# Kernel tuning notes

Measured on AMD Instinct MI355X. Metric: run time of the kernel, lower is better.

The kernel has to match this reference:

```python
import jax, jax.numpy as jnp
import numpy as np

N0, N1, N2 = 400000, 100000, 20000   # source nodes per sampled layer; dst nodes are a prefix
E1, E2 = 1000000, 200000
IN, HID, HEADS, OUT = 128, 256, 4, 47
C = HID // HEADS
EPS = 1e-5
NEG_SLOPE = 0.2


def setup_inputs() -> dict:
    key = jax.random.key(0)
    ks = jax.random.split(key, 20)
    def rn(i, shape, s=0.1):
        return jax.random.normal(ks[i], shape, jnp.float32) * s
    inp = {}
    inp["x"] = jax.random.normal(ks[0], (N0, IN), jnp.float32)
    inp["src1"] = jax.random.randint(ks[1], (E1,), 0, N0, jnp.int32)
    inp["dst1"] = jax.random.randint(ks[2], (E1,), 0, N1, jnp.int32)
    inp["src2"] = jax.random.randint(ks[3], (E2,), 0, N1, jnp.int32)
    inp["dst2"] = jax.random.randint(ks[4], (E2,), 0, N2, jnp.int32)
    # layer 1 GAT + skip + BN
    inp["W1"] = rn(5, (IN, HID)); inp["a_src1"] = rn(6, (HEADS, C)); inp["a_dst1"] = rn(7, (HEADS, C))
    inp["b1"] = jnp.zeros((HID,), jnp.float32)
    inp["Wsk1"] = rn(8, (IN, HID)); inp["bsk1"] = jnp.zeros((HID,), jnp.float32)
    inp["g1"] = jnp.ones((HID,), jnp.float32); inp["be1"] = jnp.zeros((HID,), jnp.float32)
    # layer 2 GAT + skip + BN
    inp["W2"] = rn(9, (HID, HID)); inp["a_src2"] = rn(10, (HEADS, C)); inp["a_dst2"] = rn(11, (HEADS, C))
    inp["b2"] = jnp.zeros((HID,), jnp.float32)
    inp["Wsk2"] = rn(12, (HID, HID)); inp["bsk2"] = jnp.zeros((HID,), jnp.float32)
    inp["g2"] = jnp.ones((HID,), jnp.float32); inp["be2"] = jnp.zeros((HID,), jnp.float32)
    # MLP head
    inp["Wm1"] = rn(13, (HID, HID)); inp["bm1"] = jnp.zeros((HID,), jnp.float32)
    inp["gm"] = jnp.ones((HID,), jnp.float32); inp["bem"] = jnp.zeros((HID,), jnp.float32)
    inp["Wm2"] = rn(14, (HID, OUT)); inp["bm2"] = jnp.zeros((OUT,), jnp.float32)
    return inp


def batch_norm(x, gamma, beta):
    mu = jnp.mean(x, axis=0)
    var = jnp.mean(jnp.square(x - mu), axis=0)  # biased var, as torch BN training
    return (x - mu) * jax.lax.rsqrt(var + EPS) * gamma + beta


def edge_softmax(logits, dst, n_dst):
    # logits: [E, H]; softmax over incoming edges per destination node
    m = jax.ops.segment_max(logits, dst, num_segments=n_dst)
    m = jax.lax.stop_gradient(jnp.where(jnp.isfinite(m), m, 0.0))
    e = jnp.exp(logits - m[dst])
    s = jax.ops.segment_sum(e, dst, num_segments=n_dst)
    return e / (s[dst] + 1e-16)


def gat_layer(x, n_dst, src, dst, W, a_src, a_dst, b, Wsk, bsk, gamma, beta):
    # GATConv (PyG, shared src/dst linear since in_channels is int) on bipartite (x, x[:n_dst])
    xp = (x @ W).reshape(-1, HEADS, C)                       # [N, H, C]
    al_s = jnp.einsum('nhc,hc->nh', xp, a_src)               # [N, H]
    al_d = jnp.einsum('nhc,hc->nh', xp[:n_dst], a_dst)       # [n_dst, H]
    logits = jax.nn.leaky_relu(al_s[src] + al_d[dst], NEG_SLOPE)   # [E, H]
    alpha = edge_softmax(logits, dst, n_dst)                 # [E, H]
    msg = xp[src] * alpha[:, :, None]                        # [E, H, C]
    out = jax.ops.segment_sum(msg, dst, num_segments=n_dst).reshape(n_dst, HID) + b
    out = out + x[:n_dst] @ Wsk + bsk                        # skip connection
    return jax.nn.elu(batch_norm(out, gamma, beta))          # dropout omitted (eval)


def reference(x, src1, dst1, src2, dst2,
              W1, a_src1, a_dst1, b1, Wsk1, bsk1, g1, be1,
              W2, a_src2, a_dst2, b2, Wsk2, bsk2, g2, be2,
              Wm1, bm1, gm, bem, Wm2, bm2):
    h = gat_layer(x, N1, src1, dst1, W1, a_src1, a_dst1, b1, Wsk1, bsk1, g1, be1)
    h = gat_layer(h, N2, src2, dst2, W2, a_src2, a_dst2, b2, Wsk2, bsk2, g2, be2)
    # MLP head: Linear -> BN -> ReLU -> (Dropout) -> Linear
    h = jax.nn.relu(batch_norm(h @ Wm1 + bm1, gm, bem))
    return h @ Wm2 + bm2                                     # logits [N2, OUT]
```

## Files before the change

kernel.cpp:

```cpp
#include <hip/hip_runtime.h>
#include <math.h>

constexpr int kN0 = 400000, kN1 = 100000, kN2 = 20000;
constexpr int kE1 = 1000000, kE2 = 200000;
constexpr int kIN = 128, kHID = 256, kOUT = 47;
constexpr float kEPS = 1e-5f, kNEG = 0.2f;

#define DEV static __device__ __forceinline__

typedef __attribute__((ext_vector_type(8))) short short8;
typedef __attribute__((ext_vector_type(4))) float f32x4;

DEV float b2f(unsigned short u) { return __uint_as_float(((unsigned)u) << 16); }
DEV unsigned short f2bf(float f) {
    unsigned u = __float_as_uint(f);
    unsigned r = (u + 0x7fffu + ((u >> 16) & 1u)) >> 16;
    return (unsigned short)r;
}
DEV float lrelu(float v) { return v > 0.f ? v : kNEG * v; }

DEV void gload_lds16(const void* g, void* l) {
    __builtin_amdgcn_global_load_lds(
        (const __attribute__((address_space(1))) void*)g,
        (__attribute__((address_space(3))) void*)l, 16, 0, 0);
}

__global__ void zero_f32(float* __restrict__ p, int n) {
    int i = blockIdx.x * blockDim.x + threadIdx.x;
    int st = gridDim.x * blockDim.x;
    for (; i < n; i += st) p[i] = 0.f;
}

__global__ void prep_weights(const float* __restrict__ W1, const float* __restrict__ as1,
                             const float* __restrict__ ad1,
                             const float* __restrict__ W2, const float* __restrict__ as2,
                             const float* __restrict__ ad2,
                             const float* __restrict__ Wsk1, const float* __restrict__ Wsk2,
                             const float* __restrict__ Wm1,
                             unsigned short* __restrict__ v1t, unsigned short* __restrict__ v2t,
                             unsigned short* __restrict__ Wcat1t,
                             unsigned short* __restrict__ Wcat2t,
                             unsigned short* __restrict__ Wm1t) {
    int i = blockIdx.x * blockDim.x + threadIdx.x;
    if (i < 2048) {
        int j = i >> 7, k = i & 127;
        float s = 0.f;
        if (j < 8) {
            int h = j & 3;
            const float* a = (j >= 4) ? ad1 : as1;
            for (int c = 0; c < 64; ++c) s += W1[(size_t)k * 256 + h * 64 + c] * a[h * 64 + c];
        }
        v1t[i] = f2bf(s);
        return;
    }
    i -= 2048;
    if (i < 4096) {
        int j = i >> 8, k = i & 255;
        float s = 0.f;
        if (j < 8) {
            int h = j & 3;
            const float* a = (j >= 4) ? ad2 : as2;
            for (int c = 0; c < 64; ++c) s += W2[(size_t)k * 256 + h * 64 + c] * a[h * 64 + c];
        }
        v2t[i] = f2bf(s);
        return;
    }
    i -= 4096;
    if (i < 163840) {
        int n = i / 640, k = i % 640;
        float v;
        if (k < 512) { int h = k >> 7, kin = k & 127; v = ((n >> 6) == h) ? W1[(size_t)kin * 256 + n] : 0.f; }
        else v = Wsk1[(size_t)(k - 512) * 256 + n];
        Wcat1t[i] = f2bf(v);
        return;
    }
    i -= 163840;
    if (i < 327680) {
        int n = i / 1280, k = i % 1280;
        float v;
        if (k < 1024) { int h = k >> 8, kin = k & 255; v = ((n >> 6) == h) ? W2[(size_t)kin * 256 + n] : 0.f; }
        else v = Wsk2[(size_t)(k - 1024) * 256 + n];
        Wcat2t[i] = f2bf(v);
        return;
    }
    i -= 327680;
    if (i < 65536) {
        int n = i >> 8, k = i & 255;
        Wm1t[i] = f2bf(Wm1[(size_t)k * 256 + n]);
    }
}

__global__ __launch_bounds__(256) void conv_als_mfma(const float* __restrict__ x,
                                                     const unsigned short* __restrict__ v1t,
                                                     unsigned short* __restrict__ xb,
                                                     float* __restrict__ als,
                                                     float* __restrict__ ald) {
    int wid = threadIdx.x >> 6, lane = threadIdx.x & 63;
    int l15 = lane & 15, l4 = lane >> 4;
    short8 bfr[4];
    #pragma unroll
    for (int ks = 0; ks < 4; ++ks)
        bfr[ks] = *reinterpret_cast<const short8*>(&v1t[l15 * 128 + ks * 32 + l4 * 8]);

    const int ntile = kN0 / 16;
    int nw = gridDim.x * 4;
    for (int t = blockIdx.x * 4 + wid; t < ntile; t += nw) {
        int base = t * 16;
        int r = base + l15;
        f32x4 acc = (f32x4){0.f, 0.f, 0.f, 0.f};
        #pragma unroll
        for (int ks = 0; ks < 4; ++ks) {
            size_t o = (size_t)r * 128 + ks * 32 + l4 * 8;
            float4 xa = *reinterpret_cast<const float4*>(&x[o]);
            float4 xc = *reinterpret_cast<const float4*>(&x[o + 4]);
            short8 af;
            af[0] = (short)f2bf(xa.x); af[1] = (short)f2bf(xa.y);
            af[2] = (short)f2bf(xa.z); af[3] = (short)f2bf(xa.w);
            af[4] = (short)f2bf(xc.x); af[5] = (short)f2bf(xc.y);
            af[6] = (short)f2bf(xc.z); af[7] = (short)f2bf(xc.w);
            *reinterpret_cast<short8*>(&xb[o]) = af;
            acc = __builtin_amdgcn_mfma_f32_16x16x32_bf16(af, bfr[ks], acc, 0, 0, 0);
        }
        if (l15 < 8) {
            #pragma unroll
            for (int i = 0; i < 4; ++i) {
                int node = base + l4 * 4 + i;
                if (l15 < 4) als[(size_t)node * 4 + l15] = acc[i];
                else if (node < kN1) ald[(size_t)node * 4 + (l15 - 4)] = acc[i];
            }
        }
    }
}

__global__ __launch_bounds__(256) void bn_mfma(const unsigned short* __restrict__ X,
                                               const float* __restrict__ stats,
                                               const float* __restrict__ gamma,
                                               const float* __restrict__ beta,
                                               unsigned short* __restrict__ outb,
                                               const unsigned short* __restrict__ v2t,
                                               float* __restrict__ als,
                                               float* __restrict__ ald,
                                               int M, int Ndst) {
    __shared__ float smu[256], ssc[256], ssh[256];
    {
        int c = threadIdx.x;
        float invM = 1.f / (float)M;
        float mu = stats[c] * invM;
        float var = stats[256 + c] * invM - mu * mu;
        smu[c] = mu;
        ssc[c] = rsqrtf(var + kEPS) * gamma[c];
        ssh[c] = beta[c];
    }
    __syncthreads();

    int wid = threadIdx.x >> 6, lane = threadIdx.x & 63;
    int l15 = lane & 15, l4 = lane >> 4;
    short8 bfr[8];
    #pragma unroll
    for (int ks = 0; ks < 8; ++ks)
        bfr[ks] = *reinterpret_cast<const short8*>(&v2t[l15 * 256 + ks * 32 + l4 * 8]);

    const int ntile = M / 16;
    int nw = gridDim.x * 4;
    for (int t = blockIdx.x * 4 + wid; t < ntile; t += nw) {
        int base = t * 16;
        int r = base + l15;
        f32x4 acc = (f32x4){0.f, 0.f, 0.f, 0.f};
        #pragma unroll
        for (int ks = 0; ks < 8; ++ks) {
            int c0 = ks * 32 + l4 * 8;
            size_t o = (size_t)r * 256 + c0;
            short8 xr = *reinterpret_cast<const short8*>(&X[o]);
            float4 mua = *reinterpret_cast<const float4*>(&smu[c0]);
            float4 muc = *reinterpret_cast<const float4*>(&smu[c0 + 4]);
            float4 sca = *reinterpret_cast<const float4*>(&ssc[c0]);
            float4 scc = *reinterpret_cast<const float4*>(&ssc[c0 + 4]);
            float4 sha = *reinterpret_cast<const float4*>(&ssh[c0]);
            float4 shc = *reinterpret_cast<const float4*>(&ssh[c0 + 4]);
            float v[8];
            v[0] = (b2f((unsigned short)xr[0]) - mua.x) * sca.x + sha.x;
            v[1] = (b2f((unsigned short)xr[1]) - mua.y) * sca.y + sha.y;
            v[2] = (b2f((unsigned short)xr[2]) - mua.z) * sca.z + sha.z;
            v[3] = (b2f((unsigned short)xr[3]) - mua.w) * sca.w + sha.w;
            v[4] = (b2f((unsigned short)xr[4]) - muc.x) * scc.x + shc.x;
            v[5] = (b2f((unsigned short)xr[5]) - muc.y) * scc.y + shc.y;
            v[6] = (b2f((unsigned short)xr[6]) - muc.z) * scc.z + shc.z;
            v[7] = (b2f((unsigned short)xr[7]) - muc.w) * scc.w + shc.w;
            short8 af;
            #pragma unroll
            for (int i = 0; i < 8; ++i) {
                float tv = v[i] > 0.f ? v[i] : expm1f(v[i]);
                af[i] = (short)f2bf(tv);
            }
            *reinterpret_cast<short8*>(&outb[o]) = af;
            acc = __builtin_amdgcn_mfma_f32_16x16x32_bf16(af, bfr[ks], acc, 0, 0, 0);
        }
        if (l15 < 8) {
            #pragma unroll
            for (int i = 0; i < 4; ++i) {
                int node = base + l4 * 4 + i;
                if (l15 < 4) als[(size_t)node * 4 + l15] = acc[i];
                else if (node < Ndst) ald[(size_t)node * 4 + (l15 - 4)] = acc[i];
            }
        }
    }
}

__global__ void hist_both(const int* __restrict__ dst1, int* __restrict__ cnt1, int E1,
                          const int* __restrict__ dst2, int* __restrict__ cnt2, int E2) {
    int e = blockIdx.x * blockDim.x + threadIdx.x;
    if (e < E1) atomicAdd(&cnt1[dst1[e]], 1);
    else if (e - E1 < E2) atomicAdd(&cnt2[dst2[e - E1]], 1);
}

__global__ __launch_bounds__(256) void scan_block_both(const int* __restrict__ cnt1, int n1,
                                                       int* __restrict__ offs1, int* __restrict__ bsum1, int nb1,
                                                       const int* __restrict__ cnt2, int n2,
                                                       int* __restrict__ offs2, int* __restrict__ bsum2) {
    const int* counts; int n; int* offs; int* bsum; int b;
    if ((int)blockIdx.x < nb1) { counts = cnt1; n = n1; offs = offs1; bsum = bsum1; b = blockIdx.x; }
    else { counts = cnt2; n = n2; offs = offs2; bsum = bsum2; b = blockIdx.x - nb1; }
    __shared__ int sh[256];
    int tid = threadIdx.x;
    int base = b * 1024 + tid * 4;
    int c0 = (base + 0 < n) ? counts[base + 0] : 0;
    int c1 = (base + 1 < n) ? counts[base + 1] : 0;
    int c2 = (base + 2 < n) ? counts[base + 2] : 0;
    int c3 = (base + 3 < n) ? counts[base + 3] : 0;
    int tot = c0 + c1 + c2 + c3;
    sh[tid] = tot;
    __syncthreads();
    for (int o = 1; o < 256; o <<= 1) {
        int t = (tid >= o) ? sh[tid - o] : 0;
        __syncthreads();
        sh[tid] += t;
        __syncthreads();
    }
    int excl = sh[tid] - tot;
    if (base + 0 < n) offs[base + 0] = excl;
    if (base + 1 < n) offs[base + 1] = excl + c0;
    if (base + 2 < n) offs[base + 2] = excl + c0 + c1;
    if (base + 3 < n) offs[base + 3] = excl + c0 + c1 + c2;
    if (tid == 255) bsum[b] = sh[255];
}

__global__ __launch_bounds__(256) void scan_bsums_both(const int* __restrict__ bsum1,
                                                       int* __restrict__ bscan1, int nb1,
                                                       const int* __restrict__ bsum2,
                                                       int* __restrict__ bscan2, int nb2) {
    __shared__ int sh[256];
    int tid = threadIdx.x;
    int v = (tid < nb1) ? bsum1[tid] : 0;
    sh[tid] = v;
    __syncthreads();
    for (int o = 1; o < 256; o <<= 1) {
        int t = (tid >= o) ? sh[tid - o] : 0;
        __syncthreads();
        sh[tid] += t;
        __syncthreads();
    }
    if (tid < nb1) bscan1[tid] = sh[tid] - v;
    __syncthreads();
    int v2 = (tid < nb2) ? bsum2[tid] : 0;
    sh[tid] = v2;
    __syncthreads();
    for (int o = 1; o < 256; o <<= 1) {
        int t = (tid >= o) ? sh[tid - o] : 0;
        __syncthreads();
        sh[tid] += t;
        __syncthreads();
    }
    if (tid < nb2) bscan2[tid] = sh[tid] - v2;
}

__global__ void scan_add_both(int* __restrict__ offs1, const int* __restrict__ bscan1,
                              const int* __restrict__ cnt1, int n1,
                              int* __restrict__ offs2, const int* __restrict__ bscan2,
                              const int* __restrict__ cnt2, int n2) {
    int i = blockIdx.x * blockDim.x + threadIdx.x;
    if (i < n1) {
        int v = offs1[i] + bscan1[i >> 10];
        offs1[i] = v;
        if (i == n1 - 1) offs1[n1] = v + cnt1[i];
    } else {
        int j = i - n1;
        if (j < n2) {
            int v = offs2[j] + bscan2[j >> 10];
            offs2[j] = v;
            if (j == n2 - 1) offs2[n2] = v + cnt2[j];
        }
    }
}

__global__ void csr_scatter_w(const int* __restrict__ dst, const int* __restrict__ src,
                              const int* __restrict__ offs,
                              const float* __restrict__ als, const float* __restrict__ ald,
                              int* __restrict__ cur, int* __restrict__ srcs,
                              float4* __restrict__ wbuf, int E) {
    int e = blockIdx.x * blockDim.x + threadIdx.x;
    if (e >= E) return;
    int d = dst[e], s = src[e];
    int pos = offs[d] + atomicAdd(&cur[d], 1);
    srcs[pos] = s;
    float4 a = *reinterpret_cast<const float4*>(&als[(size_t)s * 4]);
    float4 b = *reinterpret_cast<const float4*>(&ald[(size_t)d * 4]);
    float4 w;
    w.x = expf(lrelu(a.x + b.x));
    w.y = expf(lrelu(a.y + b.y));
    w.z = expf(lrelu(a.z + b.z));
    w.w = expf(lrelu(a.w + b.w));
    wbuf[pos] = w;
}

template <bool OUTBF, bool STATS>
__global__ __launch_bounds__(256) void gemm_pipe(const unsigned short* __restrict__ A1, int K1,
                                                 const unsigned short* __restrict__ A2, int K2,
                                                 const unsigned short* __restrict__ Bt,
                                                 void* __restrict__ Cv,
                                                 const float* __restrict__ bias1,
                                                 const float* __restrict__ bias2,
                                                 float* __restrict__ stats,
                                                 int M, int N, int rs, int kwin) {
    __shared__ unsigned short SH[4][128 * 64];
    const int tid = threadIdx.x;
    const int wid = tid >> 6, lane = tid & 63;
    const int wr = wid >> 1, wc = wid & 1;
    const int l15 = lane & 15, l4 = lane >> 4;
    const int m0 = blockIdx.y * 128, n0 = blockIdx.x * 128;
    const int rsub = lane >> 3;
    const int kslot = (lane & 7) ^ rsub;
    const int KB = K1 + K2;
    const int nwin = kwin >> 6;
    const int nt = nwin + (K2 >> 6);
    const int wbase = n0 * rs;

    auto stage = [&](int buf, int t) {
        const unsigned short* Asrc; int ka, lda, gk;
        if (t < nwin) { gk = wbase + (t << 6); Asrc = A1; ka = gk; lda = K1; }
        else { int t2 = t - nwin; gk = K1 + (t2 << 6); Asrc = A2; ka = t2 << 6; lda = K2; }
        #pragma unroll
        for (int c = 0; c < 4; ++c) {
            int q = wid * 4 + c;
            int rowA = m0 + q * 8 + rsub; if (rowA > M - 1) rowA = M - 1;
            gload_lds16(Asrc + (size_t)rowA * lda + ka + kslot * 8, &SH[buf][q * 512]);
            int rowB = n0 + q * 8 + rsub;
            gload_lds16(Bt + (size_t)rowB * KB + gk + kslot * 8, &SH[2 + buf][q * 512]);
        }
    };

    f32x4 acc[4][4];
    #pragma unroll
    for (int i = 0; i < 4; ++i)
        #pragma unroll
        for (int j = 0; j < 4; ++j) acc[i][j] = (f32x4){0.f, 0.f, 0.f, 0.f};

    stage(0, 0);
    __syncthreads();
    for (int t = 0; t < nt; ++t) {
        if (t + 1 < nt) stage((t + 1) & 1, t + 1);
        int b = t & 1;
        short8 af[2][4], bf[2][4];
        #pragma unroll
        for (int kk = 0; kk < 2; ++kk) {
            #pragma unroll
            for (int mi = 0; mi < 4; ++mi) {
                int row = wr * 64 + mi * 16 + l15;
                af[kk][mi] = *reinterpret_cast<const short8*>(
                    &SH[b][row * 64 + (((kk * 4 + l4) ^ (row & 7)) << 3)]);
            }
            #pragma unroll
            for (int ni = 0; ni < 4; ++ni) {
                int row = wc * 64 + ni * 16 + l15;
                bf[kk][ni] = *reinterpret_cast<const short8*>(
                    &SH[2 + b][row * 64 + (((kk * 4 + l4) ^ (row & 7)) << 3)]);
            }
        }
        #pragma unroll
        for (int kk = 0; kk < 2; ++kk)
            #pragma unroll
            for (int mi = 0; mi < 4; ++mi)
                #pragma unroll
                for (int ni = 0; ni < 4; ++ni)
                    acc[mi][ni] = __builtin_amdgcn_mfma_f32_16x16x32_bf16(
                        af[kk][mi], bf[kk][ni], acc[mi][ni], 0, 0, 0);
        __syncthreads();
    }

    float csum[4] = {0.f, 0.f, 0.f, 0.f}, csq[4] = {0.f, 0.f, 0.f, 0.f};
    unsigned short* LB = (unsigned short*)SH;
    float* LF = (float*)SH;
    #pragma unroll
    for (int mi = 0; mi < 4; ++mi) {
        int lrow0 = wr * 64 + mi * 16 + l4 * 4;
        #pragma unroll
        for (int ni = 0; ni < 4; ++ni) {
            int lcol = wc * 64 + ni * 16 + l15;
            int col = n0 + lcol;
            float badd = 0.f;
            if (bias1) badd += bias1[col];
            if (bias2) badd += bias2[col];
            f32x4 v = acc[mi][ni];
            #pragma unroll
            for (int i = 0; i < 4; ++i) {
                float o = v[i] + badd;
                if (STATS && (m0 + lrow0 + i) < M) { csum[ni] += o; csq[ni] += o * o; }
                if (OUTBF) LB[(lrow0 + i) * 128 + lcol] = f2bf(o);
                else LF[(lrow0 + i) * 128 + lcol] = o;
            }
        }
    }
    if (STATS) {
        #pragma unroll
        for (int ni = 0; ni < 4; ++ni) {
            float s = csum[ni], q = csq[ni];
            s += __shfl_xor(s, 16, 64); q += __shfl_xor(q, 16, 64);
            s += __shfl_xor(s, 32, 64); q += __shfl_xor(q, 32, 64);
            if (l4 == 0) {
                int col = n0 + wc * 64 + ni * 16 + l15;
                atomicAdd(&stats[col], s);
                atomicAdd(&stats[256 + col], q);
            }
        }
    }
    __syncthreads();
    if (OUTBF) {
        unsigned short* Cb = (unsigned short*)Cv;
        #pragma unroll
        for (int it = 0; it < 8; ++it) {
            int lin = (it * 256 + tid) * 8;
            int r = lin >> 7, c0 = lin & 127;
            int gr = m0 + r;
            if (gr < M)
                *reinterpret_cast<short8*>(&Cb[(size_t)gr * N + n0 + c0]) =
                    *reinterpret_cast<const short8*>(&LB[lin]);
        }
    } else {
        float* Cf = (float*)Cv;
        #pragma unroll
        for (int it = 0; it < 16; ++it) {
            int lin = (it * 256 + tid) * 4;
            int r = lin >> 7, c0 = lin & 127;
            int gr = m0 + r;
            if (gr < M)
                *reinterpret_cast<float4*>(&Cf[(size_t)gr * N + n0 + c0]) =
                    *reinterpret_cast<const float4*>(&LF[lin]);
        }
    }
}

__global__ __launch_bounds__(256) void fused_agg1(const unsigned short* __restrict__ xb,
                                                  const float4* __restrict__ wbuf,
                                                  const int* __restrict__ srcs,
                                                  const int* __restrict__ offs,
                                                  unsigned short* __restrict__ Agg, int Ndst) {
    int d = blockIdx.x * 4 + (threadIdx.x >> 6);
    if (d >= Ndst) return;
    int lane = threadIdx.x & 63;
    int beg = offs[d], end = offs[d + 1];
    float ac[4][2] = {};
    float se0 = 0.f, se1 = 0.f, se2 = 0.f, se3 = 0.f;

    auto edge = [&](int i) {
        int s = srcs[i];
        float4 w = wbuf[i];
        unsigned xv = *reinterpret_cast<const unsigned*>(&xb[(size_t)s * 128 + lane * 2]);
        se0 += w.x; se1 += w.y; se2 += w.z; se3 += w.w;
        float fx = b2f((unsigned short)(xv & 0xffff));
        float fy = b2f((unsigned short)(xv >> 16));
        ac[0][0] = fmaf(w.x, fx, ac[0][0]); ac[0][1] = fmaf(w.x, fy, ac[0][1]);
        ac[1][0] = fmaf(w.y, fx, ac[1][0]); ac[1][1] = fmaf(w.y, fy, ac[1][1]);
        ac[2][0] = fmaf(w.z, fx, ac[2][0]); ac[2][1] = fmaf(w.z, fy, ac[2][1]);
        ac[3][0] = fmaf(w.w, fx, ac[3][0]); ac[3][1] = fmaf(w.w, fy, ac[3][1]);
    };
    int i = beg;
    for (; i + 4 <= end; i += 4) { edge(i); edge(i + 1); edge(i + 2); edge(i + 3); }
    for (; i < end; ++i) edge(i);

    float inv0 = 1.f / (se0 + 1e-16f), inv1 = 1.f / (se1 + 1e-16f);
    float inv2 = 1.f / (se2 + 1e-16f), inv3 = 1.f / (se3 + 1e-16f);
    unsigned short* row = Agg + (size_t)d * 512;
    ushort2 o;
    o.x = f2bf(ac[0][0] * inv0); o.y = f2bf(ac[0][1] * inv0);
    *reinterpret_cast<ushort2*>(&row[0 * 128 + lane * 2]) = o;
    o.x = f2bf(ac[1][0] * inv1); o.y = f2bf(ac[1][1] * inv1);
    *reinterpret_cast<ushort2*>(&row[1 * 128 + lane * 2]) = o;
    o.x = f2bf(ac[2][0] * inv2); o.y = f2bf(ac[2][1] * inv2);
    *reinterpret_cast<ushort2*>(&row[2 * 128 + lane * 2]) = o;
    o.x = f2bf(ac[3][0] * inv3); o.y = f2bf(ac[3][1] * inv3);
    *reinterpret_cast<ushort2*>(&row[3 * 128 + lane * 2]) = o;
}

__global__ __launch_bounds__(256) void fused_agg2(const unsigned short* __restrict__ hb,
                                                  const float4* __restrict__ wbuf,
                                                  const int* __restrict__ srcs,
                                                  const int* __restrict__ offs,
                                                  unsigned short* __restrict__ Agg, int Ndst) {
    int d = blockIdx.x * 4 + (threadIdx.x >> 6);
    if (d >= Ndst) return;
    int lane = threadIdx.x & 63;
    int beg = offs[d], end = offs[d + 1];
    float ac[4][4] = {};
    float se0 = 0.f, se1 = 0.f, se2 = 0.f, se3 = 0.f;

    auto edge = [&](int i) {
        int s = srcs[i];
        float4 w = wbuf[i];
        ushort4 xv = *reinterpret_cast<const ushort4*>(&hb[(size_t)s * 256 + lane * 4]);
        se0 += w.x; se1 += w.y; se2 += w.z; se3 += w.w;
        float f0 = b2f(xv.x), f1 = b2f(xv.y), f2 = b2f(xv.z), f3 = b2f(xv.w);
        ac[0][0] = fmaf(w.x, f0, ac[0][0]); ac[0][1] = fmaf(w.x, f1, ac[0][1]);
        ac[0][2] = fmaf(w.x, f2, ac[0][2]); ac[0][3] = fmaf(w.x, f3, ac[0][3]);
        ac[1][0] = fmaf(w.y, f0, ac[1][0]); ac[1][1] = fmaf(w.y, f1, ac[1][1]);
        ac[1][2] = fmaf(w.y, f2, ac[1][2]); ac[1][3] = fmaf(w.y, f3, ac[1][3]);
        ac[2][0] = fmaf(w.z, f0, ac[2][0]); ac[2][1] = fmaf(w.z, f1, ac[2][1]);
        ac[2][2] = fmaf(w.z, f2, ac[2][2]); ac[2][3] = fmaf(w.z, f3, ac[2][3]);
        ac[3][0] = fmaf(w.w, f0, ac[3][0]); ac[3][1] = fmaf(w.w, f1, ac[3][1]);
        ac[3][2] = fmaf(w.w, f2, ac[3][2]); ac[3][3] = fmaf(w.w, f3, ac[3][3]);
    };
    int i = beg;
    for (; i + 2 <= end; i += 2) { edge(i); edge(i + 1); }
    for (; i < end; ++i) edge(i);

    float inv[4] = {1.f / (se0 + 1e-16f), 1.f / (se1 + 1e-16f),
                    1.f / (se2 + 1e-16f), 1.f / (se3 + 1e-16f)};
    unsigned short* row = Agg + (size_t)d * 1024;
    #pragma unroll
    for (int h = 0; h < 4; ++h) {
        ushort4 o;
        o.x = f2bf(ac[h][0] * inv[h]); o.y = f2bf(ac[h][1] * inv[h]);
        o.z = f2bf(ac[h][2] * inv[h]); o.w = f2bf(ac[h][3] * inv[h]);
        *reinterpret_cast<ushort4*>(&row[h * 256 + lane * 4]) = o;
    }
}

template <int ACT, bool OUTBF>
__global__ __launch_bounds__(256) void bn_rows(const float* __restrict__ X,
                                               const float* __restrict__ stats,
                                               const float* __restrict__ gamma,
                                               const float* __restrict__ beta,
                                               void* __restrict__ out, int M) {
    int wid = threadIdx.x >> 6, lane = threadIdx.x & 63;
    int nw = gridDim.x * 4;
    float4 s4 = *reinterpret_cast<const float4*>(&stats[lane * 4]);
    float4 q4 = *reinterpret_cast<const float4*>(&stats[256 + lane * 4]);
    float4 g4 = *reinterpret_cast<const float4*>(&gamma[lane * 4]);
    float4 b4 = *reinterpret_cast<const float4*>(&beta[lane * 4]);
    float invM = 1.f / (float)M;
    float mu[4] = {s4.x * invM, s4.y * invM, s4.z * invM, s4.w * invM};
    float sc[4], sh_[4] = {b4.x, b4.y, b4.z, b4.w};
    {
        float g[4] = {g4.x, g4.y, g4.z, g4.w};
        float q[4] = {q4.x, q4.y, q4.z, q4.w};
        #pragma unroll
        for (int c = 0; c < 4; ++c) {
            float var = q[c] * invM - mu[c] * mu[c];
            sc[c] = rsqrtf(var + kEPS) * g[c];
        }
    }
    for (int row = blockIdx.x * 4 + wid; row < M; row += nw) {
        float4 xv = *reinterpret_cast<const float4*>(&X[(size_t)row * 256 + lane * 4]);
        float v[4] = {xv.x, xv.y, xv.z, xv.w};
        #pragma unroll
        for (int c = 0; c < 4; ++c) {
            float t = (v[c] - mu[c]) * sc[c] + sh_[c];
            if (ACT == 0) t = t > 0.f ? t : expm1f(t);
            else t = fmaxf(t, 0.f);
            v[c] = t;
        }
        if (OUTBF) {
            ushort4 o; o.x = f2bf(v[0]); o.y = f2bf(v[1]); o.z = f2bf(v[2]); o.w = f2bf(v[3]);
            *reinterpret_cast<ushort4*>(&((unsigned short*)out)[(size_t)row * 256 + lane * 4]) = o;
        } else {
            *reinterpret_cast<float4*>(&((float*)out)[(size_t)row * 256 + lane * 4]) =
                make_float4(v[0], v[1], v[2], v[3]);
        }
    }
}

template <bool ACCUM>
__global__ __launch_bounds__(256) void gemm64(const float* __restrict__ A,
                                              const float* __restrict__ B,
                                              float* __restrict__ Cmat,
                                              const float* __restrict__ bias1,
                                              const float* __restrict__ bias2,
                                              int M, int N, int K) {
    __shared__ float As[32][68];
    __shared__ float Bs[32][68];
    const int tid = threadIdx.x;
    const int tx = tid & 15, ty = tid >> 4;
    const int m0 = blockIdx.y * 64, n0 = blockIdx.x * 64;
    float acc[4][4] = {};

    for (int k0 = 0; k0 < K; k0 += 32) {
        #pragma unroll
        for (int t = 0; t < 2; ++t) {
            int i = tid + t * 256;
            int row = i >> 3;
            int kq = (i & 7) << 2;
            float4 v = make_float4(0.f, 0.f, 0.f, 0.f);
            int gr = m0 + row;
            if (gr < M) v = *reinterpret_cast<const float4*>(&A[(size_t)gr * K + k0 + kq]);
            As[kq + 0][row] = v.x; As[kq + 1][row] = v.y;
            As[kq + 2][row] = v.z; As[kq + 3][row] = v.w;
        }
        #pragma unroll
        for (int t = 0; t < 2; ++t) {
            int i = tid + t * 256;
            int kr = i >> 4;
            int cq = (i & 15) << 2;
            #pragma unroll
            for (int j = 0; j < 4; ++j) {
                int gc = n0 + cq + j;
                Bs[kr][cq + j] = (gc < N) ? B[(size_t)(k0 + kr) * N + gc] : 0.f;
            }
        }
        __syncthreads();
        #pragma unroll
        for (int kk = 0; kk < 32; ++kk) {
            float4 a4 = *reinterpret_cast<const float4*>(&As[kk][ty << 2]);
            float4 b4 = *reinterpret_cast<const float4*>(&Bs[kk][tx << 2]);
            float a[4] = {a4.x, a4.y, a4.z, a4.w};
            float b[4] = {b4.x, b4.y, b4.z, b4.w};
            #pragma unroll
            for (int i2 = 0; i2 < 4; ++i2)
                #pragma unroll
                for (int j = 0; j < 4; ++j)
                    acc[i2][j] = fmaf(a[i2], b[j], acc[i2][j]);
        }
        __syncthreads();
    }

    #pragma unroll
    for (int i2 = 0; i2 < 4; ++i2) {
        int row = m0 + (ty << 2) + i2;
        if (row >= M) continue;
        #pragma unroll
        for (int j = 0; j < 4; ++j) {
            int col = n0 + (tx << 2) + j;
            if (col >= N) continue;
            float v = acc[i2][j];
            if (bias1) v += bias1[col];
            if (bias2) v += bias2[col];
            size_t idx = (size_t)row * N + col;
            if (ACCUM) v += Cmat[idx];
            Cmat[idx] = v;
        }
    }
}

extern "C" void kernel_launch(void* const* d_in, const int* in_sizes, int n_in,
                              void* d_out, int out_size, void* d_ws, size_t ws_size,
                              hipStream_t stream) {
    (void)in_sizes; (void)n_in; (void)out_size; (void)ws_size;

    const float* x      = (const float*)d_in[0];
    const int*   src1   = (const int*)d_in[1];
    const int*   dst1   = (const int*)d_in[2];
    const int*   src2   = (const int*)d_in[3];
    const int*   dst2   = (const int*)d_in[4];
    const float* W1     = (const float*)d_in[5];
    const float* a_src1 = (const float*)d_in[6];
    const float* a_dst1 = (const float*)d_in[7];
    const float* b1     = (const float*)d_in[8];
    const float* Wsk1   = (const float*)d_in[9];
    const float* bsk1   = (const float*)d_in[10];
    const float* g1     = (const float*)d_in[11];
    const float* be1    = (const float*)d_in[12];
    const float* W2     = (const float*)d_in[13];
    const float* a_src2 = (const float*)d_in[14];
    const float* a_dst2 = (const float*)d_in[15];
    const float* b2     = (const float*)d_in[16];
    const float* Wsk2   = (const float*)d_in[17];
    const float* bsk2   = (const float*)d_in[18];
    const float* g2     = (const float*)d_in[19];
    const float* be2    = (const float*)d_in[20];
    const float* Wm1    = (const float*)d_in[21];
    const float* bm1    = (const float*)d_in[22];
    const float* gm     = (const float*)d_in[23];
    const float* bem    = (const float*)d_in[24];
    const float* Wm2    = (const float*)d_in[25];
    const float* bm2    = (const float*)d_in[26];

    float* ws = (float*)d_ws;
    size_t off = 0;
    auto alloc = [&](size_t n) { float* p = ws + off; off += n; return p; };
    unsigned short* xb    = (unsigned short*)alloc((size_t)kN0 * 128 / 2);
    unsigned short* Agg1  = (unsigned short*)alloc((size_t)kN1 * 512 / 2);
    unsigned short* Agg2  = (unsigned short*)alloc((size_t)kN2 * 1024 / 2);
    unsigned short* h1pre = (unsigned short*)alloc((size_t)kN1 * 256 / 2);
    unsigned short* h1b   = (unsigned short*)alloc((size_t)kN1 * 256 / 2);
    float* h2             = alloc((size_t)kN2 * 256);
    unsigned short* h2b   = (unsigned short*)alloc((size_t)kN2 * 256 / 2);
    float* h3             = alloc((size_t)kN2 * 256);
    unsigned short* Wcat1t = (unsigned short*)alloc(256 * 640 / 2);
    unsigned short* Wcat2t = (unsigned short*)alloc(256 * 1280 / 2);
    unsigned short* Wm1t   = (unsigned short*)alloc(256 * 256 / 2);
    unsigned short* v1t    = (unsigned short*)alloc(16 * 128 / 2);
    unsigned short* v2t    = (unsigned short*)alloc(16 * 256 / 2);
    float4* w1buf = (float4*)alloc((size_t)kE1 * 4);
    float4* w2buf = (float4*)alloc((size_t)kE2 * 4);
    float* als1 = alloc((size_t)kN0 * 4);
    float* ald1 = alloc((size_t)kN1 * 4);
    float* als2 = alloc((size_t)kN1 * 4);
    float* ald2 = alloc((size_t)kN2 * 4);
    float* zreg = alloc(1536 + kN1 + kN1 + kN2 + kN2);
    float* stats1 = zreg, *stats2 = zreg + 512, *stats3 = zreg + 1024;
    int* cnt1 = (int*)(zreg + 1536);
    int* cur1 = cnt1 + kN1;
    int* cnt2 = cur1 + kN1;
    int* cur2 = cnt2 + kN2;
    const int nzreg = 1536 + 2 * kN1 + 2 * kN2;
    int* srcs1  = (int*)alloc(kE1);
    int* offs1  = (int*)alloc(kN1 + 4);
    int* bsum1  = (int*)alloc(128);
    int* bscan1 = (int*)alloc(128);
    int* srcs2  = (int*)alloc(kE2);
    int* offs2  = (int*)alloc(kN2 + 4);
    int* bsum2  = (int*)alloc(128);
    int* bscan2 = (int*)alloc(128);

    hipStream_t st = stream;
    const int nb1 = (kN1 + 1023) / 1024;
    const int nb2 = (kN2 + 1023) / 1024;

    prep_weights<<<(563200 + 255) / 256, 256, 0, st>>>(W1, a_src1, a_dst1, W2, a_src2, a_dst2,
                                                       Wsk1, Wsk2, Wm1,
                                                       v1t, v2t, Wcat1t, Wcat2t, Wm1t);
    zero_f32<<<512, 256, 0, st>>>(zreg, nzreg);

    conv_als_mfma<<<2048, 256, 0, st>>>(x, v1t, xb, als1, ald1);

    hist_both<<<(kE1 + kE2 + 255) / 256, 256, 0, st>>>(dst1, cnt1, kE1, dst2, cnt2, kE2);
    scan_block_both<<<nb1 + nb2, 256, 0, st>>>(cnt1, kN1, offs1, bsum1, nb1, cnt2, kN2, offs2, bsum2);
    scan_bsums_both<<<1, 256, 0, st>>>(bsum1, bscan1, nb1, bsum2, bscan2, nb2);
    scan_add_both<<<(kN1 + kN2 + 255) / 256, 256, 0, st>>>(offs1, bscan1, cnt1, kN1,
                                                           offs2, bscan2, cnt2, kN2);
    csr_scatter_w<<<(kE1 + 255) / 256, 256, 0, st>>>(dst1, src1, offs1, als1, ald1,
                                                     cur1, srcs1, w1buf, kE1);

    fused_agg1<<<(kN1 + 3) / 4, 256, 0, st>>>(xb, w1buf, srcs1, offs1, Agg1, kN1);
    gemm_pipe<true, true><<<dim3(2, (kN1 + 127) / 128), 256, 0, st>>>(
        Agg1, 512, xb, 128, Wcat1t, h1pre, b1, bsk1, stats1, kN1, 256, 2, 256);
    bn_mfma<<<1024, 256, 0, st>>>(h1pre, stats1, g1, be1, h1b, v2t, als2, ald2, kN1, kN2);

    csr_scatter_w<<<(kE2 + 255) / 256, 256, 0, st>>>(dst2, src2, offs2, als2, ald2,
                                                     cur2, srcs2, w2buf, kE2);
    fused_agg2<<<(kN2 + 3) / 4, 256, 0, st>>>(h1b, w2buf, srcs2, offs2, Agg2, kN2);
    gemm_pipe<false, true><<<dim3(2, (kN2 + 127) / 128), 256, 0, st>>>(
        Agg2, 1024, h1b, 256, Wcat2t, h2, b2, bsk2, stats2, kN2, 256, 4, 512);
    bn_rows<0, true><<<2048, 256, 0, st>>>(h2, stats2, g2, be2, h2b, kN2);

    gemm_pipe<false, true><<<dim3(2, (kN2 + 127) / 128), 256, 0, st>>>(
        h2b, 256, nullptr, 0, Wm1t, h3, bm1, nullptr, stats3, kN2, 256, 0, 256);
    bn_rows<1, false><<<2048, 256, 0, st>>>(h3, stats3, gm, bem, h3, kN2);
    gemm64<false><<<dim3(1, (kN2 + 63) / 64), 256, 0, st>>>(
        h3, Wm2, (float*)d_out, bm2, nullptr, kN2, kOUT, 256);
}
```

Before: 568.7 us.

## Fuse zeroing into prep, widen gemm_pipe to 512 threads, fuse final BN into head GEMM

```diff
diff --git a/kernel.cpp b/kernel.cpp
--- a/kernel.cpp
+++ b/kernel.cpp
@@ -25,23 +25,21 @@
         (__attribute__((address_space(3))) void*)l, 16, 0, 0);
 }
 
-__global__ void zero_f32(float* __restrict__ p, int n) {
+constexpr int kNZreg = 1536 + 2 * kN1 + 2 * kN2;
+__global__ void prep_all(const float* __restrict__ W1, const float* __restrict__ as1,
+                         const float* __restrict__ ad1,
+                         const float* __restrict__ W2, const float* __restrict__ as2,
+                         const float* __restrict__ ad2,
+                         const float* __restrict__ Wsk1, const float* __restrict__ Wsk2,
+                         const float* __restrict__ Wm1,
+                         float* __restrict__ zreg,
+                         unsigned short* __restrict__ v1t, unsigned short* __restrict__ v2t,
+                         unsigned short* __restrict__ Wcat1t,
+                         unsigned short* __restrict__ Wcat2t,
+                         unsigned short* __restrict__ Wm1t) {
     int i = blockIdx.x * blockDim.x + threadIdx.x;
-    int st = gridDim.x * blockDim.x;
-    for (; i < n; i += st) p[i] = 0.f;
-}
-
-__global__ void prep_weights(const float* __restrict__ W1, const float* __restrict__ as1,
-                             const float* __restrict__ ad1,
-                             const float* __restrict__ W2, const float* __restrict__ as2,
-                             const float* __restrict__ ad2,
-                             const float* __restrict__ Wsk1, const float* __restrict__ Wsk2,
-                             const float* __restrict__ Wm1,
-                             unsigned short* __restrict__ v1t, unsigned short* __restrict__ v2t,
-                             unsigned short* __restrict__ Wcat1t,
-                             unsigned short* __restrict__ Wcat2t,
-                             unsigned short* __restrict__ Wm1t) {
-    int i = blockIdx.x * blockDim.x + threadIdx.x;
+    if (i < kNZreg) { zreg[i] = 0.f; return; }
+    i -= kNZreg;
     if (i < 2048) {
         int j = i >> 7, k = i & 127;
         float s = 0.f;
@@ -132,6 +130,7 @@
     }
 }
 
+template <bool AL>
 __global__ __launch_bounds__(256) void bn_mfma(const unsigned short* __restrict__ X,
                                                const float* __restrict__ stats,
                                                const float* __restrict__ gamma,
@@ -156,9 +155,11 @@
     int wid = threadIdx.x >> 6, lane = threadIdx.x & 63;
     int l15 = lane & 15, l4 = lane >> 4;
     short8 bfr[8];
-    #pragma unroll
-    for (int ks = 0; ks < 8; ++ks)
-        bfr[ks] = *reinterpret_cast<const short8*>(&v2t[l15 * 256 + ks * 32 + l4 * 8]);
+    if (AL) {
+        #pragma unroll
+        for (int ks = 0; ks < 8; ++ks)
+            bfr[ks] = *reinterpret_cast<const short8*>(&v2t[l15 * 256 + ks * 32 + l4 * 8]);
+    }
 
     const int ntile = M / 16;
     int nw = gridDim.x * 4;
@@ -193,9 +194,9 @@
                 af[i] = (short)f2bf(tv);
             }
             *reinterpret_cast<short8*>(&outb[o]) = af;
-            acc = __builtin_amdgcn_mfma_f32_16x16x32_bf16(af, bfr[ks], acc, 0, 0, 0);
-        }
-        if (l15 < 8) {
+            if (AL) acc = __builtin_amdgcn_mfma_f32_16x16x32_bf16(af, bfr[ks], acc, 0, 0, 0);
+        }
+        if (AL && l15 < 8) {
             #pragma unroll
             for (int i = 0; i < 4; ++i) {
                 int node = base + l4 * 4 + i;
@@ -313,7 +314,7 @@
 }
 
 template <bool OUTBF, bool STATS>
-__global__ __launch_bounds__(256) void gemm_pipe(const unsigned short* __restrict__ A1, int K1,
+__global__ __launch_bounds__(512) void gemm_pipe(const unsigned short* __restrict__ A1, int K1,
                                                  const unsigned short* __restrict__ A2, int K2,
                                                  const unsigned short* __restrict__ Bt,
                                                  void* __restrict__ Cv,
@@ -324,7 +325,7 @@
     __shared__ unsigned short SH[4][128 * 64];
     const int tid = threadIdx.x;
     const int wid = tid >> 6, lane = tid & 63;
-    const int wr = wid >> 1, wc = wid & 1;
+    const int wr = wid >> 2, wc = wid & 3;
     const int l15 = lane & 15, l4 = lane >> 4;
     const int m0 = blockIdx.y * 128, n0 = blockIdx.x * 128;
     const int rsub = lane >> 3;
@@ -339,8 +340,8 @@
         if (t < nwin) { gk = wbase + (t << 6); Asrc = A1; ka = gk; lda = K1; }
         else { int t2 = t - nwin; gk = K1 + (t2 << 6); Asrc = A2; ka = t2 << 6; lda = K2; }
         #pragma unroll
-        for (int c = 0; c < 4; ++c) {
-            int q = wid * 4 + c;
+        for (int c = 0; c < 2; ++c) {
+            int q = wid * 2 + c;
             int rowA = m0 + q * 8 + rsub; if (rowA > M - 1) rowA = M - 1;
             gload_lds16(Asrc + (size_t)rowA * lda + ka + kslot * 8, &SH[buf][q * 512]);
             int rowB = n0 + q * 8 + rsub;
@@ -348,18 +349,18 @@
         }
     };
 
-    f32x4 acc[4][4];
+    f32x4 acc[4][2];
     #pragma unroll
     for (int i = 0; i < 4; ++i)
         #pragma unroll
-        for (int j = 0; j < 4; ++j) acc[i][j] = (f32x4){0.f, 0.f, 0.f, 0.f};
+        for (int j = 0; j < 2; ++j) acc[i][j] = (f32x4){0.f, 0.f, 0.f, 0.f};
 
     stage(0, 0);
     __syncthreads();
     for (int t = 0; t < nt; ++t) {
         if (t + 1 < nt) stage((t + 1) & 1, t + 1);
         int b = t & 1;
-        short8 af[2][4], bf[2][4];
+        short8 af[2][4], bf[2][2];
         #pragma unroll
         for (int kk = 0; kk < 2; ++kk) {
             #pragma unroll
@@ -369,8 +370,8 @@
                     &SH[b][row * 64 + (((kk * 4 + l4) ^ (row & 7)) << 3)]);
             }
             #pragma unroll
-            for (int ni = 0; ni < 4; ++ni) {
-                int row = wc * 64 + ni * 16 + l15;
+            for (int ni = 0; ni < 2; ++ni) {
+                int row = wc * 32 + ni * 16 + l15;
                 bf[kk][ni] = *reinterpret_cast<const short8*>(
                     &SH[2 + b][row * 64 + (((kk * 4 + l4) ^ (row & 7)) << 3)]);
             }
@@ -380,21 +381,21 @@
             #pragma unroll
             for (int mi = 0; mi < 4; ++mi)
                 #pragma unroll
-                for (int ni = 0; ni < 4; ++ni)
+                for (int ni = 0; ni < 2; ++ni)
                     acc[mi][ni] = __builtin_amdgcn_mfma_f32_16x16x32_bf16(
                         af[kk][mi], bf[kk][ni], acc[mi][ni], 0, 0, 0);
         __syncthreads();
     }
 
-    float csum[4] = {0.f, 0.f, 0.f, 0.f}, csq[4] = {0.f, 0.f, 0.f, 0.f};
+    float csum[2] = {0.f, 0.f}, csq[2] = {0.f, 0.f};
     unsigned short* LB = (unsigned short*)SH;
     float* LF = (float*)SH;
     #pragma unroll
     for (int mi = 0; mi < 4; ++mi) {
         int lrow0 = wr * 64 + mi * 16 + l4 * 4;
         #pragma unroll
-        for (int ni = 0; ni < 4; ++ni) {
-            int lcol = wc * 64 + ni * 16 + l15;
+        for (int ni = 0; ni < 2; ++ni) {
+            int lcol = wc * 32 + ni * 16 + l15;
             int col = n0 + lcol;
             float badd = 0.f;
             if (bias1) badd += bias1[col];
@@ -411,12 +412,12 @@
     }
     if (STATS) {
         #pragma unroll
-        for (int ni = 0; ni < 4; ++ni) {
+        for (int ni = 0; ni < 2; ++ni) {
             float s = csum[ni], q = csq[ni];
             s += __shfl_xor(s, 16, 64); q += __shfl_xor(q, 16, 64);
             s += __shfl_xor(s, 32, 64); q += __shfl_xor(q, 32, 64);
             if (l4 == 0) {
-                int col = n0 + wc * 64 + ni * 16 + l15;
+                int col = n0 + wc * 32 + ni * 16 + l15;
                 atomicAdd(&stats[col], s);
                 atomicAdd(&stats[256 + col], q);
             }
@@ -426,8 +427,8 @@
     if (OUTBF) {
         unsigned short* Cb = (unsigned short*)Cv;
         #pragma unroll
-        for (int it = 0; it < 8; ++it) {
-            int lin = (it * 256 + tid) * 8;
+        for (int it = 0; it < 4; ++it) {
+            int lin = (it * 512 + tid) * 8;
             int r = lin >> 7, c0 = lin & 127;
             int gr = m0 + r;
             if (gr < M)
@@ -437,8 +438,8 @@
     } else {
         float* Cf = (float*)Cv;
         #pragma unroll
-        for (int it = 0; it < 16; ++it) {
-            int lin = (it * 256 + tid) * 4;
+        for (int it = 0; it < 8; ++it) {
+            int lin = (it * 512 + tid) * 4;
             int r = lin >> 7, c0 = lin & 127;
             int gr = m0 + r;
             if (gr < M)
@@ -533,60 +534,28 @@
     }
 }
 
-template <int ACT, bool OUTBF>
-__global__ __launch_bounds__(256) void bn_rows(const float* __restrict__ X,
-                                               const float* __restrict__ stats,
-                                               const float* __restrict__ gamma,
-                                               const float* __restrict__ beta,
-                                               void* __restrict__ out, int M) {
-    int wid = threadIdx.x >> 6, lane = threadIdx.x & 63;
-    int nw = gridDim.x * 4;
-    float4 s4 = *reinterpret_cast<const float4*>(&stats[lane * 4]);
-    float4 q4 = *reinterpret_cast<const float4*>(&stats[256 + lane * 4]);
-    float4 g4 = *reinterpret_cast<const float4*>(&gamma[lane * 4]);
-    float4 b4 = *reinterpret_cast<const float4*>(&beta[lane * 4]);
-    float invM = 1.f / (float)M;
-    float mu[4] = {s4.x * invM, s4.y * invM, s4.z * invM, s4.w * invM};
-    float sc[4], sh_[4] = {b4.x, b4.y, b4.z, b4.w};
-    {
-        float g[4] = {g4.x, g4.y, g4.z, g4.w};
-        float q[4] = {q4.x, q4.y, q4.z, q4.w};
-        #pragma unroll
-        for (int c = 0; c < 4; ++c) {
-            float var = q[c] * invM - mu[c] * mu[c];
-            sc[c] = rsqrtf(var + kEPS) * g[c];
-        }
-    }
-    for (int row = blockIdx.x * 4 + wid; row < M; row += nw) {
-        float4 xv = *reinterpret_cast<const float4*>(&X[(size_t)row * 256 + lane * 4]);
-        float v[4] = {xv.x, xv.y, xv.z, xv.w};
-        #pragma unroll
-        for (int c = 0; c < 4; ++c) {
-            float t = (v[c] - mu[c]) * sc[c] + sh_[c];
-            if (ACT == 0) t = t > 0.f ? t : expm1f(t);
-            else t = fmaxf(t, 0.f);
-            v[c] = t;
-        }
-        if (OUTBF) {
-            ushort4 o; o.x = f2bf(v[0]); o.y = f2bf(v[1]); o.z = f2bf(v[2]); o.w = f2bf(v[3]);
-            *reinterpret_cast<ushort4*>(&((unsigned short*)out)[(size_t)row * 256 + lane * 4]) = o;
-        } else {
-            *reinterpret_cast<float4*>(&((float*)out)[(size_t)row * 256 + lane * 4]) =
-                make_float4(v[0], v[1], v[2], v[3]);
-        }
-    }
-}
-
-template <bool ACCUM>
-__global__ __launch_bounds__(256) void gemm64(const float* __restrict__ A,
-                                              const float* __restrict__ B,
-                                              float* __restrict__ Cmat,
-                                              const float* __restrict__ bias1,
-                                              const float* __restrict__ bias2,
-                                              int M, int N, int K) {
+__global__ __launch_bounds__(256) void gemm64_bn(const unsigned short* __restrict__ A,
+                                                 const float* __restrict__ B,
+                                                 float* __restrict__ Cmat,
+                                                 const float* __restrict__ bias,
+                                                 const float* __restrict__ stats,
+                                                 const float* __restrict__ gamma,
+                                                 const float* __restrict__ beta,
+                                                 int M, int N, int K) {
     __shared__ float As[32][68];
     __shared__ float Bs[32][68];
+    __shared__ float bnsc[256], bnsh[256];
     const int tid = threadIdx.x;
+    {
+        int c = tid;
+        float invM = 1.f / (float)M;
+        float mu = stats[c] * invM;
+        float var = stats[256 + c] * invM - mu * mu;
+        float sc = rsqrtf(var + kEPS) * gamma[c];
+        bnsc[c] = sc;
+        bnsh[c] = beta[c] - mu * sc;
+    }
+    __syncthreads();
     const int tx = tid & 15, ty = tid >> 4;
     const int m0 = blockIdx.y * 64, n0 = blockIdx.x * 64;
     float acc[4][4] = {};
@@ -597,11 +566,16 @@
             int i = tid + t * 256;
             int row = i >> 3;
             int kq = (i & 7) << 2;
-            float4 v = make_float4(0.f, 0.f, 0.f, 0.f);
+            ushort4 u = make_ushort4(0, 0, 0, 0);
             int gr = m0 + row;
-            if (gr < M) v = *reinterpret_cast<const float4*>(&A[(size_t)gr * K + k0 + kq]);
-            As[kq + 0][row] = v.x; As[kq + 1][row] = v.y;
-            As[kq + 2][row] = v.z; As[kq + 3][row] = v.w;
+            if (gr < M) u = *reinterpret_cast<const ushort4*>(&A[(size_t)gr * K + k0 + kq]);
+            #pragma unroll
+            for (int j = 0; j < 4; ++j) {
+                int k = k0 + kq + j;
+                unsigned short uv = (j == 0) ? u.x : (j == 1) ? u.y : (j == 2) ? u.z : u.w;
+                float v = b2f(uv) * bnsc[k] + bnsh[k];
+                As[kq + j][row] = fmaxf(v, 0.f);
+            }
         }
         #pragma unroll
         for (int t = 0; t < 2; ++t) {
@@ -638,12 +612,7 @@
         for (int j = 0; j < 4; ++j) {
             int col = n0 + (tx << 2) + j;
             if (col >= N) continue;
-            float v = acc[i2][j];
-            if (bias1) v += bias1[col];
-            if (bias2) v += bias2[col];
-            size_t idx = (size_t)row * N + col;
-            if (ACCUM) v += Cmat[idx];
-            Cmat[idx] = v;
+            Cmat[(size_t)row * N + col] = acc[i2][j] + bias[col];
         }
     }
 }
@@ -689,9 +658,9 @@
     unsigned short* Agg2  = (unsigned short*)alloc((size_t)kN2 * 1024 / 2);
     unsigned short* h1pre = (unsigned short*)alloc((size_t)kN1 * 256 / 2);
     unsigned short* h1b   = (unsigned short*)alloc((size_t)kN1 * 256 / 2);
-    float* h2             = alloc((size_t)kN2 * 256);
+    unsigned short* h2pre = (unsigned short*)alloc((size_t)kN2 * 256 / 2);
     unsigned short* h2b   = (unsigned short*)alloc((size_t)kN2 * 256 / 2);
-    float* h3             = alloc((size_t)kN2 * 256);
+    unsigned short* h3pre = (unsigned short*)alloc((size_t)kN2 * 256 / 2);
     unsigned short* Wcat1t = (unsigned short*)alloc(256 * 640 / 2);
     unsigned short* Wcat2t = (unsigned short*)alloc(256 * 1280 / 2);
     unsigned short* Wm1t   = (unsigned short*)alloc(256 * 256 / 2);
@@ -703,13 +672,12 @@
     float* ald1 = alloc((size_t)kN1 * 4);
     float* als2 = alloc((size_t)kN1 * 4);
     float* ald2 = alloc((size_t)kN2 * 4);
-    float* zreg = alloc(1536 + kN1 + kN1 + kN2 + kN2);
+    float* zreg = alloc(kNZreg);
     float* stats1 = zreg, *stats2 = zreg + 512, *stats3 = zreg + 1024;
     int* cnt1 = (int*)(zreg + 1536);
     int* cur1 = cnt1 + kN1;
     int* cnt2 = cur1 + kN1;
     int* cur2 = cnt2 + kN2;
-    const int nzreg = 1536 + 2 * kN1 + 2 * kN2;
     int* srcs1  = (int*)alloc(kE1);
     int* offs1  = (int*)alloc(kN1 + 4);
     int* bsum1  = (int*)alloc(128);
@@ -723,10 +691,9 @@
     const int nb1 = (kN1 + 1023) / 1024;
     const int nb2 = (kN2 + 1023) / 1024;
 
-    prep_weights<<<(563200 + 255) / 256, 256, 0, st>>>(W1, a_src1, a_dst1, W2, a_src2, a_dst2,
-                                                       Wsk1, Wsk2, Wm1,
-                                                       v1t, v2t, Wcat1t, Wcat2t, Wm1t);
-    zero_f32<<<512, 256, 0, st>>>(zreg, nzreg);
+    prep_all<<<(kNZreg + 563200 + 255) / 256, 256, 0, st>>>(
+        W1, a_src1, a_dst1, W2, a_src2, a_dst2, Wsk1, Wsk2, Wm1,
+        zreg, v1t, v2t, Wcat1t, Wcat2t, Wm1t);
 
     conv_als_mfma<<<2048, 256, 0, st>>>(x, v1t, xb, als1, ald1);
 
@@ -739,20 +706,20 @@
                                                      cur1, srcs1, w1buf, kE1);
 
     fused_agg1<<<(kN1 + 3) / 4, 256, 0, st>>>(xb, w1buf, srcs1, offs1, Agg1, kN1);
-    gemm_pipe<true, true><<<dim3(2, (kN1 + 127) / 128), 256, 0, st>>>(
+    gemm_pipe<true, true><<<dim3(2, (kN1 + 127) / 128), 512, 0, st>>>(
         Agg1, 512, xb, 128, Wcat1t, h1pre, b1, bsk1, stats1, kN1, 256, 2, 256);
-    bn_mfma<<<1024, 256, 0, st>>>(h1pre, stats1, g1, be1, h1b, v2t, als2, ald2, kN1, kN2);
+    bn_mfma<true><<<1024, 256, 0, st>>>(h1pre, stats1, g1, be1, h1b, v2t, als2, ald2, kN1, kN2);
 
     csr_scatter_w<<<(kE2 + 255) / 256, 256, 0, st>>>(dst2, src2, offs2, als2, ald2,
                                                      cur2, srcs2, w2buf, kE2);
     fused_agg2<<<(kN2 + 3) / 4, 256, 0, st>>>(h1b, w2buf, srcs2, offs2, Agg2, kN2);
-    gemm_pipe<false, true><<<dim3(2, (kN2 + 127) / 128), 256, 0, st>>>(
-        Agg2, 1024, h1b, 256, Wcat2t, h2, b2, bsk2, stats2, kN2, 256, 4, 512);
-    bn_rows<0, true><<<2048, 256, 0, st>>>(h2, stats2, g2, be2, h2b, kN2);
-
-    gemm_pipe<false, true><<<dim3(2, (kN2 + 127) / 128), 256, 0, st>>>(
-        h2b, 256, nullptr, 0, Wm1t, h3, bm1, nullptr, stats3, kN2, 256, 0, 256);
-    bn_rows<1, false><<<2048, 256, 0, st>>>(h3, stats3, gm, bem, h3, kN2);
-    gemm64<false><<<dim3(1, (kN2 + 63) / 64), 256, 0, st>>>(
-        h3, Wm2, (float*)d_out, bm2, nullptr, kN2, kOUT, 256);
-}
+    gemm_pipe<true, true><<<dim3(2, (kN2 + 127) / 128), 512, 0, st>>>(
+        Agg2, 1024, h1b, 256, Wcat2t, h2pre, b2, bsk2, stats2, kN2, 256, 4, 512);
+    bn_mfma<false><<<1024, 256, 0, st>>>(h2pre, stats2, g2, be2, h2b, nullptr, nullptr, nullptr,
+                                         kN2, 0);
+
+    gemm_pipe<true, true><<<dim3(2, (kN2 + 127) / 128), 512, 0, st>>>(
+        h2b, 256, nullptr, 0, Wm1t, h3pre, bm1, nullptr, stats3, kN2, 256, 0, 256);
+    gemm64_bn<<<dim3(1, (kN2 + 63) / 64), 256, 0, st>>>(
+        h3pre, Wm2, (float*)d_out, bm2, stats3, gm, bem, kN2, kOUT, 256);
+}
```

New measurement: 542.2 us. 4.7% less time.
